# Kernel tuning notes

Hardware: AMD Instinct MI355X
Metric: run time of the kernel (lower is better)

The kernel has to match this reference:

```python
import jax, jax.numpy as jnp
import numpy as np

B, S, H = 1, 1024, 2048          # batch, seq, hidden_size
I = 7168                          # intermediate_size
E = 8                             # num_local_experts
TOP_K = 2                         # num_experts_per_tok
R = int(I * H * 0.1 / (I + H))    # delta_low_rank = 159
SCALE = 0.02


def setup_inputs() -> dict:
    key = jax.random.key(0)
    ks = jax.random.split(key, 12)
    f = jnp.float32
    return {
        "x": jax.random.normal(ks[0], (B, S, H), dtype=f),
        "gate_w": jax.random.normal(ks[1], (E, H), dtype=f) * SCALE,
        "Wm1": jax.random.normal(ks[2], (I, H), dtype=f) * SCALE,  # Wmean1 (gate proj)
        "Wm2": jax.random.normal(ks[3], (H, I), dtype=f) * SCALE,  # Wmean2 (down proj)
        "Wm3": jax.random.normal(ks[4], (I, H), dtype=f) * SCALE,  # Wmean3 (up proj)
        "du1": jax.random.normal(ks[5], (E, I, R), dtype=f) * SCALE,
        "dv1": jax.random.normal(ks[6], (E, R, H), dtype=f) * SCALE,
        "du2": jax.random.normal(ks[7], (E, H, R), dtype=f) * SCALE,
        "dv2": jax.random.normal(ks[8], (E, R, I), dtype=f) * SCALE,
        "du3": jax.random.normal(ks[9], (E, I, R), dtype=f) * SCALE,
        "dv3": jax.random.normal(ks[10], (E, R, H), dtype=f) * SCALE,
    }


def reference(x, gate_w, Wm1, Wm2, Wm3, du1, dv1, du2, dv2, du3, dv3):
    b, s, h = x.shape
    hs = x.reshape(-1, h)                                  # [T, H]

    # --- router ---
    router_logits = hs @ gate_w.T                          # [T, E]
    probs = jax.nn.softmax(router_logits.astype(jnp.float32), axis=-1)
    top_w, top_i = jax.lax.top_k(probs, TOP_K)             # [T, K]
    top_w = top_w / jnp.sum(top_w, axis=-1, keepdims=True)
    # dense combine weights [T, E]: weight of expert e for token t (0 if not selected)
    comb = jnp.sum(jax.nn.one_hot(top_i, E, dtype=top_w.dtype) * top_w[..., None], axis=1)
    comb = comb.astype(hs.dtype)

    # --- shared mean weights (computed once per token) ---
    base_gate = hs @ Wm1.T                                 # [T, I]
    base_up = hs @ Wm3.T                                   # [T, I]

    # --- per-expert low-rank deltas ---
    t1 = jnp.einsum('th,erh->ter', hs, dv1)                # [T, E, R]
    gate = base_gate[:, None, :] + jnp.einsum('ter,eir->tei', t1, du1)  # [T, E, I]
    t3 = jnp.einsum('th,erh->ter', hs, dv3)
    up = base_up[:, None, :] + jnp.einsum('ter,eir->tei', t3, du3)      # [T, E, I]

    hmid = jax.nn.silu(gate) * up                          # [T, E, I]

    out = jnp.einsum('tei,hi->teh', hmid, Wm2)             # shared down proj
    t2 = jnp.einsum('tei,eri->ter', hmid, dv2)
    out = out + jnp.einsum('ter,ehr->teh', t2, du2)        # [T, E, H]

    final = jnp.einsum('te,teh->th', comb, out).reshape(b, s, h)
    return final, router_logits
```

## Files before the change

### kernel.cpp

```cpp
#include <hip/hip_runtime.h>

#define T_TOK 1024
#define H_DIM 2048
#define I_DIM 7168
#define E_NUM 8
#define R_RANK 159
#define RP 160
#define P_PAIRS 2048

#define CH_X    262144L
#define CH_W    1835008L
#define CH_DV13 325632L
#define CH_DV2  1139712L
#define CH_DU13 1146880L
#define CH_DU2  327680L

typedef __attribute__((ext_vector_type(8))) short short8;
typedef __attribute__((ext_vector_type(4))) float f32x4;

__device__ __forceinline__ ushort f2b(float f) {
  uint u = __float_as_uint(f);
  uint r = (u + 0x7FFFu + ((u >> 16) & 1u)) >> 16;
  return (ushort)r;
}
__device__ __forceinline__ float b2f(ushort u) {
  return __uint_as_float(((uint)u) << 16);
}
__device__ __forceinline__ short8 pack8(float4 a, float4 b) {
  short8 o;
  o[0] = (short)f2b(a.x); o[1] = (short)f2b(a.y); o[2] = (short)f2b(a.z); o[3] = (short)f2b(a.w);
  o[4] = (short)f2b(b.x); o[5] = (short)f2b(b.y); o[6] = (short)f2b(b.z); o[7] = (short)f2b(b.w);
  return o;
}
__device__ __forceinline__ short8 zero8() {
  short8 z;
#pragma unroll
  for (int q = 0; q < 8; ++q) z[q] = 0;
  return z;
}
__device__ __forceinline__ int swzofs(int row, int g) { return (g ^ ((row >> 1) & 3)) * 8; }

#define GLOAD(gptr, lptr) \
  __builtin_amdgcn_global_load_lds((const __attribute__((address_space(1))) void*)(gptr), \
                                   (__attribute__((address_space(3))) void*)(lptr), 16, 0, 0)

__global__ __launch_bounds__(256) void router_kernel(
    const float* __restrict__ x, const float* __restrict__ gw,
    float* __restrict__ logits, float* __restrict__ comb,
    int* __restrict__ sel_e) {
  int wave = threadIdx.x >> 6, lane = threadIdx.x & 63;
  int t = blockIdx.x * 4 + wave;
  const float* xr = x + (long)t * H_DIM;
  float acc[8] = {0.f,0.f,0.f,0.f,0.f,0.f,0.f,0.f};
  for (int h = lane * 4; h < H_DIM; h += 256) {
    const float4 xv = *(const float4*)&xr[h];
#pragma unroll
    for (int e = 0; e < 8; ++e) {
      const float4 gv = *(const float4*)&gw[e * H_DIM + h];
      acc[e] += xv.x * gv.x + xv.y * gv.y + xv.z * gv.z + xv.w * gv.w;
    }
  }
#pragma unroll
  for (int off = 32; off > 0; off >>= 1)
#pragma unroll
    for (int e = 0; e < 8; ++e) acc[e] += __shfl_down(acc[e], off);
  if (lane == 0) {
#pragma unroll
    for (int e = 0; e < 8; ++e) logits[(long)t * 8 + e] = acc[e];
    int i0 = 0;
    for (int e = 1; e < 8; ++e) if (acc[e] > acc[i0]) i0 = e;
    int i1 = (i0 == 0) ? 1 : 0;
    for (int e = 0; e < 8; ++e) if (e != i0 && acc[e] > acc[i1]) i1 = e;
    float ee = __expf(acc[i1] - acc[i0]);
    float w0 = 1.f / (1.f + ee), w1 = ee / (1.f + ee);
    for (int e = 0; e < 8; ++e) comb[t * 8 + e] = 0.f;
    comb[t * 8 + i0] = w0;
    comb[t * 8 + i1] = w1;
    sel_e[t * 2] = i0;
    sel_e[t * 2 + 1] = i1;
  }
}

__global__ __launch_bounds__(256) void setup_kernel(
    const int* __restrict__ sel_e, const float* __restrict__ comb,
    int* __restrict__ cnt, int* __restrict__ seg,
    int* __restrict__ tok, float* __restrict__ wrow, int* __restrict__ row_of) {
  __shared__ int sc[8];
  __shared__ int sseg[8];
  __shared__ int scur[8];
  const int tid = threadIdx.x;
  if (tid < 8) sc[tid] = 0;
  __syncthreads();
  for (int i = tid; i < T_TOK * 2; i += 256) atomicAdd(&sc[sel_e[i]], 1);
  __syncthreads();
  if (tid == 0) {
    int s = 0;
    for (int e = 0; e < 8; ++e) { cnt[e] = sc[e]; seg[e] = s; sseg[e] = s; s += sc[e]; }
    seg[8] = s;
  }
  if (tid < 8) scur[tid] = 0;
  __syncthreads();
  for (int t = tid; t < T_TOK; t += 256) {
#pragma unroll
    for (int k = 0; k < 2; ++k) {
      int e = sel_e[t * 2 + k];
      int pos = atomicAdd(&scur[e], 1);
      int row = sseg[e] + pos;
      tok[row] = t;
      wrow[row] = comb[t * 8 + e];
      row_of[t * 2 + k] = row;
    }
  }
}

__device__ __forceinline__ void castchunk(const float* __restrict__ s, ushort* __restrict__ d, long c) {
  const float4 a = *(const float4*)&s[c * 8];
  const float4 b = *(const float4*)&s[c * 8 + 4];
  *(short8*)&d[c * 8] = pack8(a, b);
}
__device__ __forceinline__ void padchunk(const float* __restrict__ s, ushort* __restrict__ d, long c) {
  long row = c / 20;
  int c0 = (int)(c % 20) * 8;
  short8 o;
#pragma unroll
  for (int j = 0; j < 8; ++j) {
    int cc = c0 + j;
    o[j] = (cc < R_RANK) ? (short)f2b(s[row * R_RANK + cc]) : (short)0;
  }
  *(short8*)&d[row * RP + c0] = o;
}

__global__ void megacast_kernel(
    const float* __restrict__ x, const float* __restrict__ Wm1, const float* __restrict__ Wm3,
    const float* __restrict__ dv1, const float* __restrict__ dv3,
    const float* __restrict__ du1, const float* __restrict__ du3, const float* __restrict__ du2,
    ushort* __restrict__ xb, ushort* __restrict__ w1b, ushort* __restrict__ w3b,
    ushort* __restrict__ dv1b, ushort* __restrict__ dv3b,
    ushort* __restrict__ du1b, ushort* __restrict__ du3b, ushort* __restrict__ du2b) {
  const long TOT = CH_W * 2 + CH_DU13 * 2 + CH_DU2 + CH_DV13 * 2 + CH_X;
  for (long c0 = (long)blockIdx.x * blockDim.x + threadIdx.x; c0 < TOT;
       c0 += (long)gridDim.x * blockDim.x) {
    long c = c0;
    if (c < CH_W)    { castchunk(Wm1, w1b, c); continue; }  c -= CH_W;
    if (c < CH_W)    { castchunk(Wm3, w3b, c); continue; }  c -= CH_W;
    if (c < CH_DU13) { padchunk(du1, du1b, c); continue; }  c -= CH_DU13;
    if (c < CH_DU13) { padchunk(du3, du3b, c); continue; }  c -= CH_DU13;
    if (c < CH_DU2)  { padchunk(du2, du2b, c); continue; }  c -= CH_DU2;
    if (c < CH_DV13) { castchunk(dv1, dv1b, c); continue; } c -= CH_DV13;
    if (c < CH_DV13) { castchunk(dv3, dv3b, c); continue; } c -= CH_DV13;
    castchunk(x, xb, c);
  }
}

__global__ void cast2_kernel(const float* __restrict__ Wm2, const float* __restrict__ dv2,
                             ushort* __restrict__ w2b, ushort* __restrict__ dv2b) {
  const long TOT = CH_W + CH_DV2;
  for (long c0 = (long)blockIdx.x * blockDim.x + threadIdx.x; c0 < TOT;
       c0 += (long)gridDim.x * blockDim.x) {
    long c = c0;
    if (c < CH_W) { castchunk(Wm2, w2b, c); continue; }
    c -= CH_W;
    castchunk(dv2, dv2b, c);
  }
}

__global__ void padcast8_kernel(const float* __restrict__ src, ushort* __restrict__ dst, long rows) {
  long n8 = rows * (RP / 8);
  long idx = (long)blockIdx.x * blockDim.x + threadIdx.x;
  long stride = (long)gridDim.x * blockDim.x;
  for (long i = idx; i < n8; i += stride) padchunk(src, dst, i);
}

__global__ void hcomb_kernel(const ushort* __restrict__ hmid, const int* __restrict__ row_of,
                             ushort* __restrict__ hc) {
  long idx = (long)blockIdx.x * blockDim.x + threadIdx.x;
  long total = (long)T_TOK * I_DIM / 8;
  if (idx >= total) return;
  long i = idx * 8;
  int t = (int)(i / I_DIM);
  int col = (int)(i % I_DIM);
  int r0 = row_of[t * 2], r1 = row_of[t * 2 + 1];
  const short8 a = *(const short8*)&hmid[(long)r0 * I_DIM + col];
  const short8 b = *(const short8*)&hmid[(long)r1 * I_DIM + col];
  short8 o;
#pragma unroll
  for (int j = 0; j < 8; ++j)
    o[j] = (short)f2b(b2f((ushort)a[j]) + b2f((ushort)b[j]));
  *(short8*)&hc[i] = o;
}

__global__ void finalfix_kernel(float* __restrict__ out, const ushort* __restrict__ delta,
                                const int* __restrict__ row_of) {
  long idx = (long)blockIdx.x * blockDim.x + threadIdx.x;
  long total = (long)T_TOK * H_DIM / 4;
  if (idx >= total) return;
  long i = idx * 4;
  int t = (int)(i / H_DIM);
  int col = (int)(i % H_DIM);
  int r0 = row_of[t * 2], r1 = row_of[t * 2 + 1];
  float4 d = *(float4*)&out[i];
  d.x += b2f(delta[(long)r0 * H_DIM + col + 0]) + b2f(delta[(long)r1 * H_DIM + col + 0]);
  d.y += b2f(delta[(long)r0 * H_DIM + col + 1]) + b2f(delta[(long)r1 * H_DIM + col + 1]);
  d.z += b2f(delta[(long)r0 * H_DIM + col + 2]) + b2f(delta[(long)r1 * H_DIM + col + 2]);
  d.w += b2f(delta[(long)r0 * H_DIM + col + 3]) + b2f(delta[(long)r1 * H_DIM + col + 3]);
  *(float4*)&out[i] = d;
}

__global__ void finalfixA_kernel(float* __restrict__ out, const float* __restrict__ dp,
                                 const ushort* __restrict__ delta, const int* __restrict__ row_of) {
  long idx = (long)blockIdx.x * blockDim.x + threadIdx.x;
  long total = (long)T_TOK * H_DIM / 4;
  if (idx >= total) return;
  long i = idx * 4;
  int t = (int)(i / H_DIM);
  int col = (int)(i % H_DIM);
  int r0 = row_of[t * 2], r1 = row_of[t * 2 + 1];
  const long plane = (long)T_TOK * H_DIM;
  float4 s = *(const float4*)&dp[i];
#pragma unroll
  for (int k = 1; k < 4; ++k) {
    const float4 q = *(const float4*)&dp[k * plane + i];
    s.x += q.x; s.y += q.y; s.z += q.z; s.w += q.w;
  }
  s.x += b2f(delta[(long)r0 * H_DIM + col + 0]) + b2f(delta[(long)r1 * H_DIM + col + 0]);
  s.y += b2f(delta[(long)r0 * H_DIM + col + 1]) + b2f(delta[(long)r1 * H_DIM + col + 1]);
  s.z += b2f(delta[(long)r0 * H_DIM + col + 2]) + b2f(delta[(long)r1 * H_DIM + col + 2]);
  s.w += b2f(delta[(long)r0 * H_DIM + col + 3]) + b2f(delta[(long)r1 * H_DIM + col + 3]);
  *(float4*)&out[i] = s;
}

template <int KS>
__global__ void reduce_cast_kernel(const float* __restrict__ P, long plane,
                                   ushort* __restrict__ out, long n) {
  long i = (long)blockIdx.x * blockDim.x + threadIdx.x;
  if (i >= n) return;
  float s = 0.f;
#pragma unroll
  for (int k = 0; k < KS; ++k) s += P[(long)k * plane + i];
  out[i] = f2b(s);
}

__global__ void reduce2_kernel(const float* __restrict__ p1, const float* __restrict__ p3,
                               ushort* __restrict__ t1g, ushort* __restrict__ t3g, long n) {
  long i = (long)blockIdx.x * blockDim.x + threadIdx.x;
  if (i >= 2 * n) return;
  const float* P = (i < n) ? p1 : p3;
  ushort* o = (i < n) ? t1g : t3g;
  long ii = (i < n) ? i : i - n;
  float s = 0.f;
#pragma unroll
  for (int k = 0; k < 8; ++k) s += P[(long)k * n + ii];
  o[ii] = f2b(s);
}


__device__ __forceinline__ void kloop32(
    const ushort* ar0, const ushort* ar1,
    const ushort* br0, const ushort* br1,
    int K, ushort* As, ushort* Bs,
    int tid, int lane, int wm, int wn, f32x4 acc[4][4]) {
  for (int k0 = 0; k0 < K; k0 += 32) {
    __syncthreads();
    GLOAD(ar0 + k0, &As[tid * 8]);
    GLOAD(ar1 + k0, &As[(256 + tid) * 8]);
    GLOAD(br0 + k0, &Bs[tid * 8]);
    GLOAD(br1 + k0, &Bs[(256 + tid) * 8]);
    __syncthreads();
    short8 av[4], bv[4];
#pragma unroll
    for (int mi = 0; mi < 4; ++mi) {
      int R = wm + mi * 16 + (lane & 15);
      av[mi] = *(const short8*)&As[R * 32 + swzofs(R, lane >> 4)];
    }
#pragma unroll
    for (int ni = 0; ni < 4; ++ni) {
      int R = wn + ni * 16 + (lane & 15);
      bv[ni] = *(const short8*)&Bs[R * 32 + swzofs(R, lane >> 4)];
    }
#pragma unroll
    for (int mi = 0; mi < 4; ++mi)
#pragma unroll
      for (int ni = 0; ni < 4; ++ni)
        acc[mi][ni] = __builtin_amdgcn_mfma_f32_16x16x32_bf16(av[mi], bv[ni], acc[mi][ni], 0, 0, 0);
  }
}

template <int NI>
__device__ __forceinline__ void kloop64t(
    const ushort* ar0, const ushort* ar1,
    const ushort* br0, const ushort* br1,
    int K, ushort* As, ushort* Bs,
    int tid, int lane, int wm, int wn, f32x4 acc[4][4]) {
  const int sub_r = tid >> 2;
  for (int k0 = 0; k0 < K; k0 += 64) {
    __syncthreads();
    GLOAD(ar0 + k0,      &As[tid * 8]);
    GLOAD(ar1 + k0,      &As[(256 + tid) * 8]);
    GLOAD(ar0 + k0 + 32, &As[4096 + tid * 8]);
    GLOAD(ar1 + k0 + 32, &As[4096 + (256 + tid) * 8]);
    if (NI == 4 || sub_r < 32) {
      GLOAD(br0 + k0,      &Bs[tid * 8]);
      GLOAD(br1 + k0,      &Bs[(256 + tid) * 8]);
      GLOAD(br0 + k0 + 32, &Bs[4096 + tid * 8]);
      GLOAD(br1 + k0 + 32, &Bs[4096 + (256 + tid) * 8]);
    }
    __syncthreads();
#pragma unroll
    for (int s = 0; s < 2; ++s) {
      short8 av[4], bv[NI];
#pragma unroll
      for (int mi = 0; mi < 4; ++mi) {
        int R = wm + mi * 16 + (lane & 15);
        av[mi] = *(const short8*)&As[s * 4096 + R * 32 + swzofs(R, lane >> 4)];
      }
#pragma unroll
      for (int ni = 0; ni < NI; ++ni) {
        int R = wn + ni * 16 + (lane & 15);
        bv[ni] = *(const short8*)&Bs[s * 4096 + R * 32 + swzofs(R, lane >> 4)];
      }
#pragma unroll
      for (int mi = 0; mi < 4; ++mi)
#pragma unroll
        for (int ni = 0; ni < NI; ++ni)
          acc[mi][ni] = __builtin_amdgcn_mfma_f32_16x16x32_bf16(av[mi], bv[ni], acc[mi][ni], 0, 0, 0);
    }
  }
}

__device__ __forceinline__ void epi_bf16(
    f32x4 acc[4][4], ushort* smem, int tid, int lane, int wm, int wn,
    int row0, int col0, int M, int Nvalid, int Npad, ushort* Cb, int ldc) {
  const int er = (lane >> 4) * 4, ec = lane & 15;
  __syncthreads();
#pragma unroll
  for (int mi = 0; mi < 4; ++mi)
#pragma unroll
    for (int ni = 0; ni < 4; ++ni)
#pragma unroll
      for (int j = 0; j < 4; ++j) {
        int rr = wm + mi * 16 + er + j;
        int c = wn + ni * 16 + ec;
        smem[rr * 128 + (c ^ ((rr & 7) << 3))] =
            (col0 + c < Nvalid) ? f2b(acc[mi][ni][j]) : (ushort)0;
      }
  __syncthreads();
  const int rl = tid >> 1, clb = (tid & 1) * 64;
  const int r = row0 + rl;
  if (r < M) {
    const int k8 = (rl & 7) << 3;
#pragma unroll
    for (int jj = 0; jj < 8; ++jj) {
      int cg = col0 + clb + jj * 8;
      if (cg < Npad) {
        short8 v = *(const short8*)&smem[rl * 128 + ((clb + jj * 8) ^ k8)];
        *(short8*)&Cb[(long)r * ldc + cg] = v;
      }
    }
  }
}


__global__ __launch_bounds__(256) void k_early(
    const ushort* __restrict__ xb, const ushort* __restrict__ w1b, const ushort* __restrict__ w3b,
    const ushort* __restrict__ dv1b, const ushort* __restrict__ dv3b,
    const int* __restrict__ tok, const int* __restrict__ seg, const int* __restrict__ cnt,
    ushort* __restrict__ bgate, ushort* __restrict__ bup,
    float* __restrict__ p1, float* __restrict__ p3,
    const float* __restrict__ Wm2, const float* __restrict__ dv2,
    ushort* __restrict__ w2b, ushort* __restrict__ dv2b, int docast) {
  __shared__ ushort smem[16384];
  ushort* As = smem;
  ushort* Bs = smem + 8192;
  const int b = blockIdx.x;
  const int tid = threadIdx.x;
  const int lane = tid & 63, wave = tid >> 6;
  const int wm = (wave >> 1) * 64, wn = (wave & 1) * 64;
  const int sub_r = tid >> 2, sub_c = swzofs(sub_r, tid & 3);

  if (b < 896) {
    const int z = b / 448, r448 = b % 448;
    const int xk = r448 % 56, yk = r448 / 56;
    const int row0 = yk * 128, col0 = xk * 128;
    const ushort* B = z ? w3b : w1b;
    ushort* C = z ? bup : bgate;
    const ushort* ar0 = xb + (long)(row0 + sub_r) * H_DIM + sub_c;
    const ushort* ar1 = xb + (long)(row0 + 64 + sub_r) * H_DIM + sub_c;
    const ushort* br0 = B + (long)(col0 + sub_r) * H_DIM + sub_c;
    const ushort* br1 = B + (long)(col0 + 64 + sub_r) * H_DIM + sub_c;
    f32x4 acc[4][4] = {};
    kloop64t<4>(ar0, ar1, br0, br1, H_DIM, As, Bs, tid, lane, wm, wn, acc);
    epi_bf16(acc, smem, tid, lane, wm, wn, row0, col0, T_TOK, I_DIM, I_DIM, C, I_DIM);
  } else if (b < 2944) {
    const int f = b - 896;
    const int xk = f & 1, yk = (f >> 1) & 7, zk = f >> 4;
    const int which = zk & 1;
    const int eks = zk >> 1;
    const int e = eks >> 3, ks = eks & 7;
    const int m0 = seg[e], M = cnt[e];
    const int row0 = yk * 128, col0 = xk * 128;
    if (row0 >= M) return;
    const int kbase = ks * 256;
    const ushort* Bsrc = (which ? dv3b : dv1b) + (long)e * R_RANK * H_DIM;
    float* P = which ? p3 : p1;
    int r0c = row0 + sub_r;      if (r0c > M - 1) r0c = M - 1;
    int r1c = row0 + 64 + sub_r; if (r1c > M - 1) r1c = M - 1;
    const ushort* ar0 = xb + (long)tok[m0 + r0c] * H_DIM + kbase + sub_c;
    const ushort* ar1 = xb + (long)tok[m0 + r1c] * H_DIM + kbase + sub_c;
    int q0 = col0 + sub_r;      if (q0 > R_RANK - 1) q0 = R_RANK - 1;
    int q1 = col0 + 64 + sub_r; if (q1 > R_RANK - 1) q1 = R_RANK - 1;
    const ushort* br0 = Bsrc + (long)q0 * H_DIM + kbase + sub_c;
    const ushort* br1 = Bsrc + (long)q1 * H_DIM + kbase + sub_c;
    f32x4 acc[4][4] = {};
    if (xk == 0)
      kloop64t<4>(ar0, ar1, br0, br1, 256, As, Bs, tid, lane, wm, wn, acc);
    else
      kloop64t<2>(ar0, ar1, br0, br1, 256, As, Bs, tid, lane, wm, wn, acc);
    const int er = (lane >> 4) * 4, ec = lane & 15;
    const long plane = (long)P_PAIRS * RP;
#pragma unroll
    for (int mi = 0; mi < 4; ++mi)
#pragma unroll
      for (int ni = 0; ni < 4; ++ni)
#pragma unroll
        for (int j = 0; j < 4; ++j) {
          int r = row0 + wm + mi * 16 + er + j;
          int c = col0 + wn + ni * 16 + ec;
          if (r < M && c < RP)
            P[(long)ks * plane + (long)(m0 + r) * RP + c] = (c < R_RANK) ? acc[mi][ni][j] : 0.f;
        }
  } else if (docast) {
    const long TOT = CH_W + CH_DV2;
    for (long c0 = (long)(b - 2944) * 256 + tid; c0 < TOT; c0 += 512L * 256L) {
      long c = c0;
      if (c < CH_W) { castchunk(Wm2, w2b, c); continue; }
      c -= CH_W;
      castchunk(dv2, dv2b, c);
    }
  }
}

__global__ __launch_bounds__(256) void k_phase2(
    const ushort* __restrict__ hc, const ushort* __restrict__ w2b,
    const ushort* __restrict__ hmidg, const ushort* __restrict__ dv2b,
    const int* __restrict__ seg, const int* __restrict__ cnt,
    float* __restrict__ dp, float* __restrict__ p2) {
  __shared__ ushort smem[16384];
  ushort* As = smem;
  ushort* Bs = smem + 8192;
  const int tid = threadIdx.x;
  const int lane = tid & 63, wave = tid >> 6;
  const int wm = (wave >> 1) * 64, wn = (wave & 1) * 64;
  const int sub_r = tid >> 2, sub_c = swzofs(sub_r, tid & 3);
  const int er = (lane >> 4) * 4, ec = lane & 15;

  if (blockIdx.z < 4) {
    const int ks = blockIdx.z;
    const int kbase = ks * (I_DIM / 4);
    const int row0 = blockIdx.y * 128, col0 = blockIdx.x * 128;
    const ushort* ar0 = hc + (long)(row0 + sub_r) * I_DIM + kbase + sub_c;
    const ushort* ar1 = hc + (long)(row0 + 64 + sub_r) * I_DIM + kbase + sub_c;
    const ushort* br0 = w2b + (long)(col0 + sub_r) * I_DIM + kbase + sub_c;
    const ushort* br1 = w2b + (long)(col0 + 64 + sub_r) * I_DIM + kbase + sub_c;
    f32x4 acc[4][4] = {};
    kloop64t<4>(ar0, ar1, br0, br1, I_DIM / 4, As, Bs, tid, lane, wm, wn, acc);
    float* Pk = dp + (long)ks * T_TOK * H_DIM;
#pragma unroll
    for (int mi = 0; mi < 4; ++mi)
#pragma unroll
      for (int ni = 0; ni < 4; ++ni)
#pragma unroll
        for (int j = 0; j < 4; ++j) {
          int r = row0 + wm + mi * 16 + er + j;
          int c = col0 + wn + ni * 16 + ec;
          Pk[(long)r * H_DIM + c] = acc[mi][ni][j];
        }
  } else {
    const int f = (blockIdx.z - 4) * 128 + blockIdx.y * 16 + blockIdx.x;
    const int eks = f >> 4;
    const int e = eks >> 3, ks = eks & 7;
    const int rsub = f & 15;
    const int x2 = rsub & 1, y2 = rsub >> 1;
    const int m0 = seg[e], M = cnt[e];
    const int row0 = y2 * 128, col0 = x2 * 128;
    if (row0 >= M) return;
    const int kbase = ks * (I_DIM / 8);
    int r0c = row0 + sub_r;      if (r0c > M - 1) r0c = M - 1;
    int r1c = row0 + 64 + sub_r; if (r1c > M - 1) r1c = M - 1;
    const ushort* ar0 = hmidg + (long)(m0 + r0c) * I_DIM + kbase + sub_c;
    const ushort* ar1 = hmidg + (long)(m0 + r1c) * I_DIM + kbase + sub_c;
    int q0 = col0 + sub_r;      if (q0 > R_RANK - 1) q0 = R_RANK - 1;
    int q1 = col0 + 64 + sub_r; if (q1 > R_RANK - 1) q1 = R_RANK - 1;
    const ushort* br0 = dv2b + (long)e * R_RANK * I_DIM + (long)q0 * I_DIM + kbase + sub_c;
    const ushort* br1 = dv2b + (long)e * R_RANK * I_DIM + (long)q1 * I_DIM + kbase + sub_c;
    f32x4 acc[4][4] = {};
    if (x2 == 0)
      kloop64t<4>(ar0, ar1, br0, br1, I_DIM / 8, As, Bs, tid, lane, wm, wn, acc);
    else
      kloop64t<2>(ar0, ar1, br0, br1, I_DIM / 8, As, Bs, tid, lane, wm, wn, acc);
    const long plane = (long)P_PAIRS * RP;
#pragma unroll
    for (int mi = 0; mi < 4; ++mi)
#pragma unroll
      for (int ni = 0; ni < 4; ++ni)
#pragma unroll
        for (int j = 0; j < 4; ++j) {
          int r = row0 + wm + mi * 16 + er + j;
          int c = col0 + wn + ni * 16 + ec;
          if (r < M && c < RP)
            p2[(long)ks * plane + (long)(m0 + r) * RP + c] = (c < R_RANK) ? acc[mi][ni][j] : 0.f;
        }
  }
}

__global__ __launch_bounds__(256) void k_delta(
    const ushort* __restrict__ t2g, const ushort* __restrict__ du2b,
    const int* __restrict__ seg, const int* __restrict__ cnt,
    ushort* __restrict__ deltab) {
  __shared__ ushort smem[16384];
  ushort* As = smem;
  ushort* Bs = smem + 4096;
  const int e = blockIdx.z;
  const int m0 = seg[e], M = cnt[e];
  const int row0 = blockIdx.y * 128, col0 = blockIdx.x * 128;
  if (row0 >= M) return;
  const int tid = threadIdx.x;
  const int lane = tid & 63, wave = tid >> 6;
  const int wm = (wave >> 1) * 64, wn = (wave & 1) * 64;
  const int sub_r = tid >> 2, sub_c = swzofs(sub_r, tid & 3);
  int r0c = row0 + sub_r;      if (r0c > M - 1) r0c = M - 1;
  int r1c = row0 + 64 + sub_r; if (r1c > M - 1) r1c = M - 1;
  const ushort* ar0 = t2g + (long)(m0 + r0c) * RP + sub_c;
  const ushort* ar1 = t2g + (long)(m0 + r1c) * RP + sub_c;
  const ushort* br0 = du2b + (long)e * H_DIM * RP + (long)(col0 + sub_r) * RP + sub_c;
  const ushort* br1 = du2b + (long)e * H_DIM * RP + (long)(col0 + 64 + sub_r) * RP + sub_c;
  f32x4 acc[4][4] = {};
  kloop32(ar0, ar1, br0, br1, RP, As, Bs, tid, lane, wm, wn, acc);
  epi_bf16(acc, smem, tid, lane, wm, wn, row0, col0, M, H_DIM, H_DIM,
           deltab + (long)m0 * H_DIM, H_DIM);
}

__global__ __launch_bounds__(256) void gemm_hmid(
    const ushort* __restrict__ t1g, const ushort* __restrict__ t3g,
    const ushort* __restrict__ du1b, const ushort* __restrict__ du3b,
    const ushort* __restrict__ bgate, const ushort* __restrict__ bup,
    const int* __restrict__ tok, const float* __restrict__ wrow,
    const int* __restrict__ seg, const int* __restrict__ cnt,
    ushort* __restrict__ hmid) {
  __shared__ ushort smem[16384];
  ushort* As1 = smem;
  ushort* As3 = smem + 4096;
  ushort* Bs1 = smem + 8192;
  ushort* Bs3 = smem + 12288;
  int e = blockIdx.z;
  int m0 = seg[e], M = cnt[e];
  if ((int)(blockIdx.y * 128) >= M) return;
  const ushort* A1 = t1g + (long)m0 * RP;
  const ushort* A3 = t3g + (long)m0 * RP;
  const ushort* B1 = du1b + (long)e * I_DIM * RP;
  const ushort* B3 = du3b + (long)e * I_DIM * RP;
  tok += m0; wrow += m0;
  ushort* H = hmid + (long)m0 * I_DIM;

  const int tid = threadIdx.x;
  const int lane = tid & 63, wave = tid >> 6;
  const int wm = (wave >> 1) * 64, wn = (wave & 1) * 64;
  const int row0 = blockIdx.y * 128, col0 = blockIdx.x * 128;
  const int sub_r = tid >> 2;
  const int sub_c = swzofs(sub_r, tid & 3);

  const ushort *a1r[2], *a3r[2], *b1r[2], *b3r[2];
#pragma unroll
  for (int p = 0; p < 2; ++p) {
    int r = row0 + p * 64 + sub_r; if (r > M - 1) r = M - 1;
    a1r[p] = A1 + (long)r * RP + sub_c;
    a3r[p] = A3 + (long)r * RP + sub_c;
    int q = col0 + p * 64 + sub_r; if (q > I_DIM - 1) q = I_DIM - 1;
    b1r[p] = B1 + (long)q * RP + sub_c;
    b3r[p] = B3 + (long)q * RP + sub_c;
  }

  f32x4 acc1[4][4] = {}, acc3[4][4] = {};

  for (int k0 = 0; k0 < RP; k0 += 32) {
    __syncthreads();
#pragma unroll
    for (int p = 0; p < 2; ++p) {
      GLOAD(a1r[p] + k0, &As1[(p * 256 + tid) * 8]);
      GLOAD(a3r[p] + k0, &As3[(p * 256 + tid) * 8]);
      GLOAD(b1r[p] + k0, &Bs1[(p * 256 + tid) * 8]);
      GLOAD(b3r[p] + k0, &Bs3[(p * 256 + tid) * 8]);
    }
    __syncthreads();

    short8 av1[4], av3[4], bv1[4], bv3[4];
#pragma unroll
    for (int mi = 0; mi < 4; ++mi) {
      int R = wm + mi * 16 + (lane & 15);
      int o = R * 32 + swzofs(R, lane >> 4);
      av1[mi] = *(const short8*)&As1[o];
      av3[mi] = *(const short8*)&As3[o];
    }
#pragma unroll
    for (int ni = 0; ni < 4; ++ni) {
      int R = wn + ni * 16 + (lane & 15);
      int o = R * 32 + swzofs(R, lane >> 4);
      bv1[ni] = *(const short8*)&Bs1[o];
      bv3[ni] = *(const short8*)&Bs3[o];
    }
#pragma unroll
    for (int mi = 0; mi < 4; ++mi)
#pragma unroll
      for (int ni = 0; ni < 4; ++ni) {
        acc1[mi][ni] = __builtin_amdgcn_mfma_f32_16x16x32_bf16(av1[mi], bv1[ni], acc1[mi][ni], 0, 0, 0);
        acc3[mi][ni] = __builtin_amdgcn_mfma_f32_16x16x32_bf16(av3[mi], bv3[ni], acc3[mi][ni], 0, 0, 0);
      }
  }

  const int er = (lane >> 4) * 4;
  const int ec = lane & 15;
  __syncthreads();
  ushort* Cs = smem;
#pragma unroll
  for (int mi = 0; mi < 4; ++mi)
#pragma unroll
    for (int ni = 0; ni < 4; ++ni)
#pragma unroll
      for (int j = 0; j < 4; ++j) {
        int rr = wm + mi * 16 + er + j;
        int c = wn + ni * 16 + ec;
        Cs[rr * 128 + (c ^ ((rr & 7) << 3))] = f2b(acc1[mi][ni][j]);
      }
  __syncthreads();
  const int rl = tid >> 1;
  const int clb = (tid & 1) * 64;
  const int r = row0 + rl;
  const bool rok = (r < M);
  const int t = rok ? tok[r] : 0;
  const float w = rok ? wrow[r] : 0.f;
  const int k8 = (rl & 7) << 3;
  uint svp[32];
#pragma unroll
  for (int jj = 0; jj < 8; ++jj) {
    short8 gb = zero8();
    if (rok) gb = *(const short8*)&bgate[(long)t * I_DIM + col0 + clb + jj * 8];
    short8 gv = *(const short8*)&Cs[rl * 128 + ((clb + jj * 8) ^ k8)];
#pragma unroll
    for (int q = 0; q < 8; q += 2) {
      float g0 = b2f((ushort)gv[q]) + b2f((ushort)gb[q]);
      float g1 = b2f((ushort)gv[q + 1]) + b2f((ushort)gb[q + 1]);
      float s0 = g0 / (1.f + __expf(-g0));
      float s1 = g1 / (1.f + __expf(-g1));
      svp[jj * 4 + q / 2] = (uint)f2b(s0) | ((uint)f2b(s1) << 16);
    }
  }
  __syncthreads();
#pragma unroll
  for (int mi = 0; mi < 4; ++mi)
#pragma unroll
    for (int ni = 0; ni < 4; ++ni)
#pragma unroll
      for (int j = 0; j < 4; ++j) {
        int rr = wm + mi * 16 + er + j;
        int c = wn + ni * 16 + ec;
        Cs[rr * 128 + (c ^ ((rr & 7) << 3))] = f2b(acc3[mi][ni][j]);
      }
  __syncthreads();
#pragma unroll
  for (int jj = 0; jj < 8; ++jj) {
    short8 ub = zero8();
    if (rok) ub = *(const short8*)&bup[(long)t * I_DIM + col0 + clb + jj * 8];
    short8 uv = *(const short8*)&Cs[rl * 128 + ((clb + jj * 8) ^ k8)];
    short8 o;
#pragma unroll
    for (int q = 0; q < 8; q += 2) {
      uint sp = svp[jj * 4 + q / 2];
      float u0 = b2f((ushort)uv[q]) + b2f((ushort)ub[q]);
      float u1 = b2f((ushort)uv[q + 1]) + b2f((ushort)ub[q + 1]);
      o[q]     = (short)f2b(w * b2f((ushort)(sp & 0xFFFFu)) * u0);
      o[q + 1] = (short)f2b(w * b2f((ushort)(sp >> 16)) * u1);
    }
    if (rok) *(short8*)&H[(long)r * I_DIM + col0 + clb + jj * 8] = o;
  }
}

template <int AF32, int BF32, int CBF16, int PEREXP, int AMAP>
__global__ __launch_bounds__(256) void gemm_f(
    const void* __restrict__ Ap, int lda,
    const void* __restrict__ Bp, int ldb, long Bstride,
    int M, int N, int K, int Npad,
    float* __restrict__ Cf, ushort* __restrict__ Cb, int ldc,
    const int* __restrict__ tok, const int* __restrict__ seg, const int* __restrict__ cnt) {
  __shared__ ushort smem[16384];
  ushort* As = smem;
  ushort* Bs = smem + 4096;
  const float* Af = (const float*)Ap;
  const ushort* Ab = (const ushort*)Ap;
  const float* Bf = (const float*)Bp;
  const ushort* Bb = (const ushort*)Bp;
  const int* amap = tok;
  if (PEREXP) {
    int e = blockIdx.z;
    int m0 = seg[e];
    M = cnt[e];
    if ((int)(blockIdx.y * 128) >= M) return;
    if (AMAP) {
      amap = tok + m0;
    } else {
      if (AF32) Af += (long)m0 * lda; else Ab += (long)m0 * lda;
    }
    if (BF32) Bf += (long)e * Bstride; else Bb += (long)e * Bstride;
    if (CBF16) Cb += (long)m0 * ldc; else Cf += (long)m0 * ldc;
  }
  const int tid = threadIdx.x;
  const int lane = tid & 63, wave = tid >> 6;
  const int wm = (wave >> 1) * 64, wn = (wave & 1) * 64;
  const int row0 = blockIdx.y * 128, col0 = blockIdx.x * 128;
  const int sub_r = tid >> 2;
  const int sub_c = (tid & 3) * 8;

  const float* afrow[2]; const ushort* abrow[2];
  const float* bfrow[2]; const ushort* bbrow[2];
#pragma unroll
  for (int p = 0; p < 2; ++p) {
    int r = row0 + p * 64 + sub_r; if (r > M - 1) r = M - 1;
    if (AMAP) r = amap[r];
    if (AF32) afrow[p] = Af + (long)r * lda + sub_c;
    else      abrow[p] = Ab + (long)r * lda + sub_c;
    int q = col0 + p * 64 + sub_r; if (q > N - 1) q = N - 1;
    if (BF32) bfrow[p] = Bf + (long)q * ldb + sub_c;
    else      bbrow[p] = Bb + (long)q * ldb + sub_c;
  }

  f32x4 acc[4][4] = {};

  for (int k0 = 0; k0 < K; k0 += 32) {
    float4 a0[2], a1[2], b0[2], b1[2];
    if (AF32) {
#pragma unroll
      for (int p = 0; p < 2; ++p) {
        a0[p] = *(const float4*)(afrow[p] + k0);
        a1[p] = *(const float4*)(afrow[p] + k0 + 4);
      }
    }
    if (BF32) {
#pragma unroll
      for (int p = 0; p < 2; ++p) {
        b0[p] = *(const float4*)(bfrow[p] + k0);
        b1[p] = *(const float4*)(bfrow[p] + k0 + 4);
      }
    }
    __syncthreads();
#pragma unroll
    for (int p = 0; p < 2; ++p) {
      if (AF32) {
        *(short8*)&As[(p * 256 + tid) * 8] = pack8(a0[p], a1[p]);
      } else {
        GLOAD(abrow[p] + k0, &As[(p * 256 + tid) * 8]);
      }
      if (BF32) {
        *(short8*)&Bs[(p * 256 + tid) * 8] = pack8(b0[p], b1[p]);
      } else {
        GLOAD(bbrow[p] + k0, &Bs[(p * 256 + tid) * 8]);
      }
    }
    __syncthreads();

    short8 av[4], bv[4];
#pragma unroll
    for (int mi = 0; mi < 4; ++mi)
      av[mi] = *(const short8*)&As[(wm + mi * 16 + (lane & 15)) * 32 + (lane >> 4) * 8];
#pragma unroll
    for (int ni = 0; ni < 4; ++ni)
      bv[ni] = *(const short8*)&Bs[(wn + ni * 16 + (lane & 15)) * 32 + (lane >> 4) * 8];
#pragma unroll
    for (int mi = 0; mi < 4; ++mi)
#pragma unroll
      for (int ni = 0; ni < 4; ++ni)
        acc[mi][ni] = __builtin_amdgcn_mfma_f32_16x16x32_bf16(av[mi], bv[ni], acc[mi][ni], 0, 0, 0);
  }

  const int er = (lane >> 4) * 4;
  const int ec = lane & 15;
  if (CBF16) {
    __syncthreads();
    ushort* Cs = smem;
#pragma unroll
    for (int mi = 0; mi < 4; ++mi)
#pragma unroll
      for (int ni = 0; ni < 4; ++ni)
#pragma unroll
        for (int j = 0; j < 4; ++j) {
          int rr = wm + mi * 16 + er + j;
          int c = wn + ni * 16 + ec;
          Cs[rr * 128 + (c ^ ((rr & 7) << 3))] =
              (col0 + c < N) ? f2b(acc[mi][ni][j]) : (ushort)0;
        }
    __syncthreads();
    const int rl = tid >> 1;
    const int clb = (tid & 1) * 64;
    const int r = row0 + rl;
    if (r < M) {
      const int k8 = (rl & 7) << 3;
#pragma unroll
      for (int jj = 0; jj < 8; ++jj) {
        int cg = col0 + clb + jj * 8;
        if (cg < Npad) {
          short8 v = *(const short8*)&Cs[rl * 128 + ((clb + jj * 8) ^ k8)];
          *(short8*)&Cb[(long)r * ldc + cg] = v;
        }
      }
    }
  } else {
#pragma unroll
    for (int mi = 0; mi < 4; ++mi)
#pragma unroll
      for (int ni = 0; ni < 4; ++ni)
#pragma unroll
        for (int j = 0; j < 4; ++j) {
          int r = row0 + wm + mi * 16 + er + j;
          int c = col0 + wn + ni * 16 + ec;
          if (r < M && c < Npad)
            Cf[(long)r * ldc + c] = (c < N) ? acc[mi][ni][j] : 0.f;
        }
  }
}

extern "C" void kernel_launch(void* const* d_in, const int* in_sizes, int n_in,
                              void* d_out, int out_size, void* d_ws, size_t ws_size,
                              hipStream_t stream) {
  const float* x   = (const float*)d_in[0];
  const float* gw  = (const float*)d_in[1];
  const float* Wm1 = (const float*)d_in[2];
  const float* Wm2 = (const float*)d_in[3];
  const float* Wm3 = (const float*)d_in[4];
  const float* du1 = (const float*)d_in[5];
  const float* dv1 = (const float*)d_in[6];
  const float* du2 = (const float*)d_in[7];
  const float* dv2 = (const float*)d_in[8];
  const float* du3 = (const float*)d_in[9];
  const float* dv3 = (const float*)d_in[10];

  float* out_final  = (float*)d_out;
  float* out_logits = out_final + (long)T_TOK * H_DIM;

  char* p = (char*)d_ws;
  auto alloc = [&](size_t bytes) {
    char* r = p;
    p += (bytes + 255) & ~(size_t)255;
    return r;
  };

  float* comb   = (float*)alloc((size_t)T_TOK * E_NUM * 4);
  float* wrow   = (float*)alloc((size_t)P_PAIRS * 4);
  int* cnt      = (int*)alloc(64);
  int* seg      = (int*)alloc(64);
  int* sel_e    = (int*)alloc((size_t)T_TOK * 2 * 4);
  int* tok      = (int*)alloc((size_t)P_PAIRS * 4);
  int* row_of   = (int*)alloc((size_t)T_TOK * 2 * 4);
  ushort* bgate_b = (ushort*)alloc((size_t)T_TOK * I_DIM * 2);
  ushort* bup_b   = (ushort*)alloc((size_t)T_TOK * I_DIM * 2);
  ushort* hmidg   = (ushort*)alloc((size_t)P_PAIRS * I_DIM * 2);
  ushort* t1g     = (ushort*)alloc((size_t)P_PAIRS * RP * 2);
  ushort* t3g     = (ushort*)alloc((size_t)P_PAIRS * RP * 2);
  ushort* t2g     = (ushort*)alloc((size_t)P_PAIRS * RP * 2);
  ushort* du1b    = (ushort*)alloc((size_t)E_NUM * I_DIM * RP * 2);
  ushort* du3b    = (ushort*)alloc((size_t)E_NUM * I_DIM * RP * 2);
  ushort* du2b    = (ushort*)alloc((size_t)E_NUM * H_DIM * RP * 2);
  size_t needed_B = (size_t)(p - (char*)d_ws);
  ushort* xb   = (ushort*)alloc((size_t)T_TOK * H_DIM * 2);
  ushort* w1b  = (ushort*)alloc((size_t)I_DIM * H_DIM * 2);
  ushort* w3b  = (ushort*)alloc((size_t)I_DIM * H_DIM * 2);
  ushort* dv1b = (ushort*)alloc((size_t)E_NUM * R_RANK * H_DIM * 2);
  ushort* dv3b = (ushort*)alloc((size_t)E_NUM * R_RANK * H_DIM * 2);
  size_t needed_A = (size_t)(p - (char*)d_ws);
  ushort* w2b_d  = (ushort*)alloc((size_t)I_DIM * H_DIM * 2);
  ushort* dv2b_d = (ushort*)alloc((size_t)E_NUM * R_RANK * I_DIM * 2);
  size_t needed_A2 = (size_t)(p - (char*)d_ws);

  ushort* hc     = bgate_b;
  ushort* deltab = bup_b;

  if (ws_size < needed_B) return;
  const bool planA  = (ws_size >= needed_A);
  const bool planA2 = (ws_size >= needed_A2);

  dim3 blk(256);

  router_kernel<<<T_TOK / 4, 256, 0, stream>>>(x, gw, out_logits, comb, sel_e);
  setup_kernel<<<1, 256, 0, stream>>>(sel_e, comb, cnt, seg, tok, wrow, row_of);

  if (planA) {
    ushort* w2b  = planA2 ? w2b_d  : w1b;
    ushort* dv2b = planA2 ? dv2b_d : w3b;

    megacast_kernel<<<2048, 256, 0, stream>>>(x, Wm1, Wm3, dv1, dv3, du1, du3, du2,
                                              xb, w1b, w3b, dv1b, dv3b, du1b, du3b, du2b);

    float* p1 = (float*)hmidg;
    float* p3 = p1 + (long)8 * P_PAIRS * RP;
    k_early<<<3456, blk, 0, stream>>>(xb, w1b, w3b, dv1b, dv3b, tok, seg, cnt,
                                      bgate_b, bup_b, p1, p3,
                                      Wm2, dv2, w2b, dv2b, planA2 ? 1 : 0);
    reduce2_kernel<<<2560, 256, 0, stream>>>(p1, p3, t1g, t3g, (long)P_PAIRS * RP);

    if (!planA2)
      cast2_kernel<<<1024, 256, 0, stream>>>(Wm2, dv2, w2b, dv2b);

    gemm_hmid<<<dim3(I_DIM / 128, 8, E_NUM), blk, 0, stream>>>(
        t1g, t3g, du1b, du3b, bgate_b, bup_b, tok, wrow, seg, cnt, hmidg);

    hcomb_kernel<<<(int)(((long)T_TOK * I_DIM / 8 + 255) / 256), 256, 0, stream>>>(hmidg, row_of, hc);

    float* dp = (float*)du1b;
    float* p2 = (float*)bup_b;
    k_phase2<<<dim3(H_DIM / 128, 8, 12), blk, 0, stream>>>(
        hc, w2b, hmidg, dv2b, seg, cnt, dp, p2);
    reduce_cast_kernel<8><<<1280, 256, 0, stream>>>(p2, (long)P_PAIRS * RP, t2g, (long)P_PAIRS * RP);

    k_delta<<<dim3(H_DIM / 128, 8, E_NUM), blk, 0, stream>>>(t2g, du2b, seg, cnt, deltab);

    finalfixA_kernel<<<2048, 256, 0, stream>>>(out_final, dp, deltab, row_of);
  } else {
    padcast8_kernel<<<4480, 256, 0, stream>>>(du1, du1b, (long)E_NUM * I_DIM);
    padcast8_kernel<<<4480, 256, 0, stream>>>(du3, du3b, (long)E_NUM * I_DIM);
    padcast8_kernel<<<1280, 256, 0, stream>>>(du2, du2b, (long)E_NUM * H_DIM);
    gemm_f<1, 1, 1, 0, 0><<<dim3(I_DIM / 128, T_TOK / 128, 1), blk, 0, stream>>>(
        x, H_DIM, Wm1, H_DIM, 0L, T_TOK, I_DIM, H_DIM, I_DIM,
        nullptr, bgate_b, I_DIM, nullptr, nullptr, nullptr);
    gemm_f<1, 1, 1, 0, 0><<<dim3(I_DIM / 128, T_TOK / 128, 1), blk, 0, stream>>>(
        x, H_DIM, Wm3, H_DIM, 0L, T_TOK, I_DIM, H_DIM, I_DIM,
        nullptr, bup_b, I_DIM, nullptr, nullptr, nullptr);
    gemm_f<1, 1, 1, 1, 1><<<dim3(2, 8, E_NUM), blk, 0, stream>>>(
        x, H_DIM, dv1, H_DIM, (long)R_RANK * H_DIM, 0, R_RANK, H_DIM, RP,
        nullptr, t1g, RP, tok, seg, cnt);
    gemm_f<1, 1, 1, 1, 1><<<dim3(2, 8, E_NUM), blk, 0, stream>>>(
        x, H_DIM, dv3, H_DIM, (long)R_RANK * H_DIM, 0, R_RANK, H_DIM, RP,
        nullptr, t3g, RP, tok, seg, cnt);
    gemm_hmid<<<dim3(I_DIM / 128, 8, E_NUM), blk, 0, stream>>>(
        t1g, t3g, du1b, du3b, bgate_b, bup_b, tok, wrow, seg, cnt, hmidg);
    hcomb_kernel<<<(int)(((long)T_TOK * I_DIM / 8 + 255) / 256), 256, 0, stream>>>(hmidg, row_of, hc);
    gemm_f<0, 1, 0, 0, 0><<<dim3(H_DIM / 128, T_TOK / 128, 1), blk, 0, stream>>>(
        hc, I_DIM, Wm2, I_DIM, 0L, T_TOK, H_DIM, I_DIM, H_DIM,
        out_final, nullptr, H_DIM, nullptr, nullptr, nullptr);
    gemm_f<0, 1, 1, 1, 0><<<dim3(2, 8, E_NUM), blk, 0, stream>>>(
        hmidg, I_DIM, dv2, I_DIM, (long)R_RANK * I_DIM, 0, R_RANK, I_DIM, RP,
        nullptr, t2g, RP, tok, seg, cnt);
    gemm_f<0, 0, 1, 1, 0><<<dim3(H_DIM / 128, 8, E_NUM), blk, 0, stream>>>(
        t2g, RP, du2b, RP, (long)H_DIM * RP, 0, H_DIM, RP, H_DIM,
        nullptr, deltab, H_DIM, tok, seg, cnt);
    finalfix_kernel<<<(int)(((long)T_TOK * H_DIM / 4 + 255) / 256), 256, 0, stream>>>(
        out_final, deltab, row_of);
  }
}
```

Before: 435.2 us.

## Fuse router into cast kernel and move du casts into early GEMM launch

```diff
diff --git a/kernel.cpp b/kernel.cpp
--- a/kernel.cpp
+++ b/kernel.cpp
@@ -44,12 +44,11 @@
   __builtin_amdgcn_global_load_lds((const __attribute__((address_space(1))) void*)(gptr), \
                                    (__attribute__((address_space(3))) void*)(lptr), 16, 0, 0)
 
-__global__ __launch_bounds__(256) void router_kernel(
-    const float* __restrict__ x, const float* __restrict__ gw,
-    float* __restrict__ logits, float* __restrict__ comb,
-    int* __restrict__ sel_e) {
-  int wave = threadIdx.x >> 6, lane = threadIdx.x & 63;
-  int t = blockIdx.x * 4 + wave;
+__device__ __forceinline__ void router_body(
+    int b, int tid, const float* __restrict__ x, const float* __restrict__ gw,
+    float* __restrict__ logits, float* __restrict__ comb, int* __restrict__ sel_e) {
+  int wave = tid >> 6, lane = tid & 63;
+  int t = b * 4 + wave;
   const float* xr = x + (long)t * H_DIM;
   float acc[8] = {0.f,0.f,0.f,0.f,0.f,0.f,0.f,0.f};
   for (int h = lane * 4; h < H_DIM; h += 256) {
@@ -79,6 +78,12 @@
     sel_e[t * 2] = i0;
     sel_e[t * 2 + 1] = i1;
   }
+}
+
+__global__ __launch_bounds__(256) void router_kernel(
+    const float* __restrict__ x, const float* __restrict__ gw,
+    float* __restrict__ logits, float* __restrict__ comb, int* __restrict__ sel_e) {
+  router_body(blockIdx.x, threadIdx.x, x, gw, logits, comb, sel_e);
 }
 
 __global__ __launch_bounds__(256) void setup_kernel(
@@ -130,22 +135,24 @@
   *(short8*)&d[row * RP + c0] = o;
 }
 
-__global__ void megacast_kernel(
-    const float* __restrict__ x, const float* __restrict__ Wm1, const float* __restrict__ Wm3,
+__global__ __launch_bounds__(256) void megacast2_kernel(
+    const float* __restrict__ x, const float* __restrict__ gw,
+    const float* __restrict__ Wm1, const float* __restrict__ Wm3,
     const float* __restrict__ dv1, const float* __restrict__ dv3,
-    const float* __restrict__ du1, const float* __restrict__ du3, const float* __restrict__ du2,
+    float* __restrict__ logits, float* __restrict__ comb, int* __restrict__ sel_e,
     ushort* __restrict__ xb, ushort* __restrict__ w1b, ushort* __restrict__ w3b,
-    ushort* __restrict__ dv1b, ushort* __restrict__ dv3b,
-    ushort* __restrict__ du1b, ushort* __restrict__ du3b, ushort* __restrict__ du2b) {
-  const long TOT = CH_W * 2 + CH_DU13 * 2 + CH_DU2 + CH_DV13 * 2 + CH_X;
-  for (long c0 = (long)blockIdx.x * blockDim.x + threadIdx.x; c0 < TOT;
-       c0 += (long)gridDim.x * blockDim.x) {
+    ushort* __restrict__ dv1b, ushort* __restrict__ dv3b) {
+  const int b = blockIdx.x;
+  const int tid = threadIdx.x;
+  if (b < 256) {
+    router_body(b, tid, x, gw, logits, comb, sel_e);
+    return;
+  }
+  const long TOT = CH_W * 2 + CH_DV13 * 2 + CH_X;
+  for (long c0 = (long)(b - 256) * 256 + tid; c0 < TOT; c0 += 2048L * 256L) {
     long c = c0;
     if (c < CH_W)    { castchunk(Wm1, w1b, c); continue; }  c -= CH_W;
     if (c < CH_W)    { castchunk(Wm3, w3b, c); continue; }  c -= CH_W;
-    if (c < CH_DU13) { padchunk(du1, du1b, c); continue; }  c -= CH_DU13;
-    if (c < CH_DU13) { padchunk(du3, du3b, c); continue; }  c -= CH_DU13;
-    if (c < CH_DU2)  { padchunk(du2, du2b, c); continue; }  c -= CH_DU2;
     if (c < CH_DV13) { castchunk(dv1, dv1b, c); continue; } c -= CH_DV13;
     if (c < CH_DV13) { castchunk(dv3, dv3b, c); continue; } c -= CH_DV13;
     castchunk(x, xb, c);
@@ -366,6 +373,8 @@
     const int* __restrict__ tok, const int* __restrict__ seg, const int* __restrict__ cnt,
     ushort* __restrict__ bgate, ushort* __restrict__ bup,
     float* __restrict__ p1, float* __restrict__ p3,
+    const float* __restrict__ du1, const float* __restrict__ du3, const float* __restrict__ du2,
+    ushort* __restrict__ du1b, ushort* __restrict__ du3b, ushort* __restrict__ du2b,
     const float* __restrict__ Wm2, const float* __restrict__ dv2,
     ushort* __restrict__ w2b, ushort* __restrict__ dv2b, int docast) {
   __shared__ ushort smem[16384];
@@ -377,8 +386,20 @@
   const int wm = (wave >> 1) * 64, wn = (wave & 1) * 64;
   const int sub_r = tid >> 2, sub_c = swzofs(sub_r, tid & 3);
 
-  if (b < 896) {
-    const int z = b / 448, r448 = b % 448;
+  if (b < 512) {
+    const long TOTA = CH_DU13 * 2 + CH_DU2;
+    const long TOT = docast ? (TOTA + CH_W + CH_DV2) : TOTA;
+    for (long c0 = (long)b * 256 + tid; c0 < TOT; c0 += 512L * 256L) {
+      long c = c0;
+      if (c < CH_DU13) { padchunk(du1, du1b, c); continue; }  c -= CH_DU13;
+      if (c < CH_DU13) { padchunk(du3, du3b, c); continue; }  c -= CH_DU13;
+      if (c < CH_DU2)  { padchunk(du2, du2b, c); continue; }  c -= CH_DU2;
+      if (c < CH_W)    { castchunk(Wm2, w2b, c); continue; }  c -= CH_W;
+      castchunk(dv2, dv2b, c);
+    }
+  } else if (b < 1408) {
+    const int bb = b - 512;
+    const int z = bb / 448, r448 = bb % 448;
     const int xk = r448 % 56, yk = r448 / 56;
     const int row0 = yk * 128, col0 = xk * 128;
     const ushort* B = z ? w3b : w1b;
@@ -390,8 +411,8 @@
     f32x4 acc[4][4] = {};
     kloop64t<4>(ar0, ar1, br0, br1, H_DIM, As, Bs, tid, lane, wm, wn, acc);
     epi_bf16(acc, smem, tid, lane, wm, wn, row0, col0, T_TOK, I_DIM, I_DIM, C, I_DIM);
-  } else if (b < 2944) {
-    const int f = b - 896;
+  } else {
+    const int f = b - 1408;
     const int xk = f & 1, yk = (f >> 1) & 7, zk = f >> 4;
     const int which = zk & 1;
     const int eks = zk >> 1;
@@ -428,14 +449,6 @@
           if (r < M && c < RP)
             P[(long)ks * plane + (long)(m0 + r) * RP + c] = (c < R_RANK) ? acc[mi][ni][j] : 0.f;
         }
-  } else if (docast) {
-    const long TOT = CH_W + CH_DV2;
-    for (long c0 = (long)(b - 2944) * 256 + tid; c0 < TOT; c0 += 512L * 256L) {
-      long c = c0;
-      if (c < CH_W) { castchunk(Wm2, w2b, c); continue; }
-      c -= CH_W;
-      castchunk(dv2, dv2b, c);
-    }
   }
 }
 
@@ -886,20 +899,20 @@
 
   dim3 blk(256);
 
-  router_kernel<<<T_TOK / 4, 256, 0, stream>>>(x, gw, out_logits, comb, sel_e);
-  setup_kernel<<<1, 256, 0, stream>>>(sel_e, comb, cnt, seg, tok, wrow, row_of);
-
   if (planA) {
     ushort* w2b  = planA2 ? w2b_d  : w1b;
     ushort* dv2b = planA2 ? dv2b_d : w3b;
 
-    megacast_kernel<<<2048, 256, 0, stream>>>(x, Wm1, Wm3, dv1, dv3, du1, du3, du2,
-                                              xb, w1b, w3b, dv1b, dv3b, du1b, du3b, du2b);
+    megacast2_kernel<<<2304, 256, 0, stream>>>(x, gw, Wm1, Wm3, dv1, dv3,
+                                               out_logits, comb, sel_e,
+                                               xb, w1b, w3b, dv1b, dv3b);
+    setup_kernel<<<1, 256, 0, stream>>>(sel_e, comb, cnt, seg, tok, wrow, row_of);
 
     float* p1 = (float*)hmidg;
     float* p3 = p1 + (long)8 * P_PAIRS * RP;
     k_early<<<3456, blk, 0, stream>>>(xb, w1b, w3b, dv1b, dv3b, tok, seg, cnt,
                                       bgate_b, bup_b, p1, p3,
+                                      du1, du3, du2, du1b, du3b, du2b,
                                       Wm2, dv2, w2b, dv2b, planA2 ? 1 : 0);
     reduce2_kernel<<<2560, 256, 0, stream>>>(p1, p3, t1g, t3g, (long)P_PAIRS * RP);
 
@@ -921,6 +934,8 @@
 
     finalfixA_kernel<<<2048, 256, 0, stream>>>(out_final, dp, deltab, row_of);
   } else {
+    router_kernel<<<T_TOK / 4, 256, 0, stream>>>(x, gw, out_logits, comb, sel_e);
+    setup_kernel<<<1, 256, 0, stream>>>(sel_e, comb, cnt, seg, tok, wrow, row_of);
     padcast8_kernel<<<4480, 256, 0, stream>>>(du1, du1b, (long)E_NUM * I_DIM);
     padcast8_kernel<<<4480, 256, 0, stream>>>(du3, du3b, (long)E_NUM * I_DIM);
     padcast8_kernel<<<1280, 256, 0, stream>>>(du2, du2b, (long)E_NUM * H_DIM);
```

New measurement: 439.0 us. Within noise of the previous version (+0.9%).
